# Kernel tuning notes

Measured on AMD Instinct MI355X. Metric: run time of the kernel, lower is better.

Reference implementation:

```python
import jax, jax.numpy as jnp
import numpy as np

B, N_IN, N_OUT = 16, 7000, 28000
C_IN, C_OUT, S = 64, 64, 9
NNZ = 3 * N_OUT  # ~3 source verts per upsampled vert (barycentric)


def setup_inputs() -> dict:
    key = jax.random.key(0)
    k = jax.random.split(key, 6)
    x = jax.random.normal(k[0], (B, N_IN, C_IN), dtype=jnp.float32)
    values = jax.random.uniform(k[1], (NNZ,), dtype=jnp.float32)
    row = jax.random.randint(k[2], (NNZ,), 0, N_OUT)
    col = jax.random.randint(k[3], (NNZ,), 0, N_IN)
    spiral_indices = jax.random.randint(k[4], (N_OUT, S), 0, N_OUT)
    weight = jax.random.normal(k[5], (S * C_IN, C_OUT), dtype=jnp.float32) * 0.02
    bias = jnp.zeros((C_OUT,), dtype=jnp.float32)
    return {"x": x, "values": values, "weight": weight, "bias": bias,
            "row": row, "col": col, "spiral_indices": spiral_indices}


def reference(x, values, weight, bias, row, col, spiral_indices):
    # Pool: gather source verts, scale by sparse matrix values, scatter-add to output verts
    n_out = spiral_indices.shape[0]
    gathered = x[:, col, :] * values[None, :, None]            # [B, nnz, C]
    pooled = jnp.zeros((x.shape[0], n_out, x.shape[2]), x.dtype).at[:, row, :].add(gathered)  # [B, N_out, C]
    # SpiralConv: gather spiral neighborhood, flatten, linear
    feat = pooled[:, spiral_indices.reshape(-1), :]            # [B, N_out*S, C]
    feat = feat.reshape(x.shape[0], n_out, -1)                 # [B, N_out, S*C]
    out = jax.nn.elu(jnp.einsum('bnf,fo->bno', feat, weight) + bias)
    return out
```

## Files before the change

kernel.cpp:

```cpp
#include <hip/hip_runtime.h>
#include <math.h>

#define B      16
#define N_IN   7000
#define N_OUT  28000
#define C      64
#define S      9
#define NNZ    (3 * N_OUT)
#define F      (S * C)
#define KB     (F / 32)

typedef short bf16x8 __attribute__((ext_vector_type(8)));
typedef float f32x4  __attribute__((ext_vector_type(4)));

static __device__ __forceinline__ unsigned short f2bf(float f) {
    unsigned u = __float_as_uint(f);
    u += 0x7fffu + ((u >> 16) & 1u);
    return (unsigned short)(u >> 16);
}

__global__ void hist_kernel(const int* __restrict__ row, int* __restrict__ cnt) {
    int i = blockIdx.x * 256 + threadIdx.x;
    if (i < NNZ) atomicAdd(&cnt[row[i]], 1);
}

__global__ void scan_kernel(const int* __restrict__ cnt,
                            int* __restrict__ offs, int* __restrict__ cursor) {
    __shared__ int tmp[1024];
    const int t = threadIdx.x;
    const int base = t * 28;
    const bool live = (t < 1000);

    int c[28];
    int partial = 0;
    if (live) {
        #pragma unroll
        for (int j = 0; j < 28; ++j) { c[j] = cnt[base + j]; partial += c[j]; }
    }
    tmp[t] = partial;
    __syncthreads();
    #pragma unroll
    for (int off = 1; off < 1024; off <<= 1) {
        int v = (t >= off) ? tmp[t - off] : 0;
        __syncthreads();
        tmp[t] += v;
        __syncthreads();
    }
    if (live) {
        int run = tmp[t] - partial;
        #pragma unroll
        for (int j = 0; j < 28; ++j) {
            offs[base + j]   = run;
            cursor[base + j] = run;
            run += c[j];
        }
        if (t == 999) offs[N_OUT] = run;
    }
}

__global__ void place_kernel(const int* __restrict__ row, const int* __restrict__ col,
                             const float* __restrict__ values,
                             int* __restrict__ cursor,
                             int* __restrict__ ecol, float* __restrict__ eval) {
    int i = blockIdx.x * 256 + threadIdx.x;
    if (i < NNZ) {
        int pos = atomicAdd(&cursor[row[i]], 1);
        ecol[pos] = col[i];
        eval[pos] = values[i];
    }
}

__global__ void pool_kernel(const float* __restrict__ x,
                            const int*   __restrict__ ecol,
                            const float* __restrict__ eval,
                            const int*   __restrict__ offs,
                            unsigned short* __restrict__ pooled) {
    const int bg     = blockIdx.x & 7;
    const int rowblk = blockIdx.x >> 3;
    const int wave = threadIdx.x >> 6;
    const int lane = threadIdx.x & 63;
    const int rsub = lane >> 5;
    const int bsub = (lane >> 4) & 1;
    const int sl   = lane & 15;

    const int r = rowblk * 8 + wave * 2 + rsub;
    const int b = bg + 8 * bsub;

    const int start = offs[r], end = offs[r + 1];

    float4 acc = make_float4(0.f, 0.f, 0.f, 0.f);
    const float* xb = x + (size_t)b * N_IN * C + sl * 4;

    for (int e = start; e < end; e += 4) {
        const int nn = end - e;
        int   cl[4]; float vv[4];
        #pragma unroll
        for (int j = 0; j < 4; ++j) {
            const int ee = (j < nn) ? e + j : e;
            cl[j] = ecol[ee];
            vv[j] = (j < nn) ? eval[ee] : 0.f;
        }
        float4 xv[4];
        #pragma unroll
        for (int j = 0; j < 4; ++j)
            xv[j] = *(const float4*)(xb + (size_t)cl[j] * C);
        #pragma unroll
        for (int j = 0; j < 4; ++j) {
            acc.x = fmaf(xv[j].x, vv[j], acc.x);
            acc.y = fmaf(xv[j].y, vv[j], acc.y);
            acc.z = fmaf(xv[j].z, vv[j], acc.z);
            acc.w = fmaf(xv[j].w, vv[j], acc.w);
        }
    }

    unsigned long long ov =
        (unsigned long long)f2bf(acc.x)
        | ((unsigned long long)f2bf(acc.y) << 16)
        | ((unsigned long long)f2bf(acc.z) << 32)
        | ((unsigned long long)f2bf(acc.w) << 48);
    unsigned short* dst = pooled + (size_t)bsub * (N_OUT * 512)
                        + (size_t)r * 512 + bg * 64 + sl * 4;
    __builtin_nontemporal_store(ov, (unsigned long long*)dst);
}

__global__ void packw_kernel(const float* __restrict__ w, unsigned short* __restrict__ pw) {
    const int kb   = blockIdx.x;
    const int nt   = threadIdx.x >> 6;
    const int lane = threadIdx.x & 63;
    const int lm   = lane & 15;
    const int quad = lane >> 4;

    unsigned short v[8];
    #pragma unroll
    for (int j = 0; j < 8; ++j) {
        const int k = kb * 32 + quad * 8 + j;
        const int n = nt * 16 + lm;
        v[j] = f2bf(w[(size_t)k * C + n]);
    }
    unsigned short* dst = pw + ((size_t)(kb * 4 + nt) * 64 + lane) * 8;
    #pragma unroll
    for (int j = 0; j < 8; ++j) dst[j] = v[j];
}

__global__ __launch_bounds__(512, 2)
void spiral_mfma(const unsigned short* __restrict__ pooled,
                 const bf16x8*         __restrict__ packedW,
                 const int*            __restrict__ sp,
                 const float*          __restrict__ bias,
                 float*                __restrict__ out) {
    const int Lb    = blockIdx.x;
    const int g     = Lb & 1;
    const int mtile = Lb >> 1;
    const int wave  = threadIdx.x >> 6;
    const int lane  = threadIdx.x & 63;
    const int lm    = lane & 15;
    const int quad  = lane >> 4;
    const int m_base = mtile * 32;
    const int b      = g * 8 + wave;

    __shared__ bf16x8         bw[KB * 4 * 64];
    __shared__ unsigned short apool[2][32][512];

    {
        const int t = threadIdx.x;
        #pragma unroll
        for (int i = 0; i < 9; ++i)
            bw[i * 512 + t] = packedW[i * 512 + t];
    }

    int spv[S];
    {
        const int r = m_base + (lane & 31);
        #pragma unroll
        for (int s = 0; s < S; ++s) spv[s] = sp[r * S + s];
    }

    const unsigned short* pgbase = pooled + (size_t)g * (N_OUT * 512);

    f32x4 acc[2][4];
    #pragma unroll
    for (int t = 0; t < 2; ++t)
        #pragma unroll
        for (int nt = 0; nt < 4; ++nt)
            acc[t][nt] = (f32x4){0.f, 0.f, 0.f, 0.f};

    bf16x8 ld[4];

    #pragma unroll
    for (int q = 0; q < 4; ++q) {
        const int r = __shfl(spv[0], wave * 4 + q, 64);
        ld[q] = *(const bf16x8*)(pgbase + (size_t)r * 512 + lane * 8);
    }
    #pragma unroll
    for (int q = 0; q < 4; ++q) {
        const int j = wave * 4 + q;
        *(bf16x8*)(&apool[0][j][(lane ^ (j & 7)) * 8]) = ld[q];
    }
    __syncthreads();

    #pragma unroll
    for (int s = 0; s < S; ++s) {
        const int cur = s & 1, nxt = cur ^ 1;

        if (s + 1 < S) {
            #pragma unroll
            for (int q = 0; q < 4; ++q) {
                const int r = __shfl(spv[s + 1], wave * 4 + q, 64);
                ld[q] = *(const bf16x8*)(pgbase + (size_t)r * 512 + lane * 8);
            }
        }

        #pragma unroll
        for (int half = 0; half < 2; ++half) {
            bf16x8 bb[4];
            #pragma unroll
            for (int nt = 0; nt < 4; ++nt)
                bb[nt] = bw[((s * 2 + half) * 4 + nt) * 64 + lane];
            bf16x8 aa[2];
            #pragma unroll
            for (int t = 0; t < 2; ++t) {
                const int j = t * 16 + lm;
                const int chunk = wave * 8 + (((half * 4 + quad) ^ (j & 7)));
                aa[t] = *(const bf16x8*)(&apool[cur][j][chunk * 8]);
            }
            #pragma unroll
            for (int nt = 0; nt < 4; ++nt)
                #pragma unroll
                for (int t = 0; t < 2; ++t)
                    acc[t][nt] = __builtin_amdgcn_mfma_f32_16x16x32_bf16(
                        aa[t], bb[nt], acc[t][nt], 0, 0, 0);
        }

        if (s + 1 < S) {
            #pragma unroll
            for (int q = 0; q < 4; ++q) {
                const int j = wave * 4 + q;
                *(bf16x8*)(&apool[nxt][j][(lane ^ (j & 7)) * 8]) = ld[q];
            }
        }
        __syncthreads();
    }

    #pragma unroll
    for (int nt = 0; nt < 4; ++nt) {
        const int n = nt * 16 + lm;
        const float bs = bias[n];
        #pragma unroll
        for (int t = 0; t < 2; ++t) {
            #pragma unroll
            for (int reg = 0; reg < 4; ++reg) {
                const int r = m_base + t * 16 + quad * 4 + reg;
                float v = acc[t][nt][reg] + bs;
                v = v > 0.f ? v : (__expf(v) - 1.0f);
                __builtin_nontemporal_store(v,
                    out + ((size_t)b * N_OUT + r) * C + n);
            }
        }
    }
}

extern "C" void kernel_launch(void* const* d_in, const int* in_sizes, int n_in,
                              void* d_out, int out_size, void* d_ws, size_t ws_size,
                              hipStream_t stream) {
    const float* x      = (const float*)d_in[0];
    const float* values = (const float*)d_in[1];
    const float* weight = (const float*)d_in[2];
    const float* bias   = (const float*)d_in[3];
    const int*   row    = (const int*)d_in[4];
    const int*   col    = (const int*)d_in[5];
    const int*   sp     = (const int*)d_in[6];
    float*       out    = (float*)d_out;

    char* ws = (char*)d_ws;
    size_t off = 0;
    unsigned short* pooled  = (unsigned short*)(ws + off); off += (size_t)B * N_OUT * C * 2;
    unsigned short* packedW = (unsigned short*)(ws + off); off += (size_t)KB * 4 * 64 * 8 * 2;
    int*   offs   = (int*)(ws + off); off += ((size_t)(N_OUT + 1) * 4 + 124) / 128 * 128;
    int*   cursor = (int*)(ws + off); off += (size_t)N_OUT * 4 + 128;
    int*   cnt    = (int*)(ws + off); off += (size_t)N_OUT * 4 + 128;
    int*   ecol   = (int*)(ws + off); off += (size_t)NNZ * 4;
    float* eval   = (float*)(ws + off); off += (size_t)NNZ * 4;

    (void)hipMemsetAsync(cnt, 0, (size_t)N_OUT * 4, stream);
    hist_kernel <<<(NNZ + 255) / 256, 256, 0, stream>>>(row, cnt);
    scan_kernel <<<1, 1024, 0, stream>>>(cnt, offs, cursor);
    place_kernel<<<(NNZ + 255) / 256, 256, 0, stream>>>(row, col, values, cursor, ecol, eval);

    packw_kernel<<<KB, 256, 0, stream>>>(weight, packedW);

    pool_kernel<<<3500 * 8, 256, 0, stream>>>(x, ecol, eval, offs, pooled);

    spiral_mfma<<<875 * 2, 512, 0, stream>>>(pooled,
        reinterpret_cast<const bf16x8*>(packedW), sp, bias, out);
}
```

Before: 300.3 us.

## Convert x to bf16 before pooling and stream weights per spiral step

Adds a kernel that converts x to bf16 so the pooling gather reads half the bytes. In the spiral GEMM, the full weight matrix is no longer held in LDS; one 8KB slice per spiral step is double-buffered alongside the A tiles, which shrinks LDS use so launch bounds can ask for 4 blocks per CU. The cost is an extra launch plus a full read and write of x, and weight slices now come from global memory every step. It also loses some pooled precision because inputs are rounded to bf16 before accumulation.

```diff
diff --git a/kernel.cpp b/kernel.cpp
--- a/kernel.cpp
+++ b/kernel.cpp
@@ -17,6 +17,9 @@
     unsigned u = __float_as_uint(f);
     u += 0x7fffu + ((u >> 16) & 1u);
     return (unsigned short)(u >> 16);
+}
+static __device__ __forceinline__ float bf2f(unsigned short s) {
+    return __uint_as_float((unsigned)s << 16);
 }
 
 __global__ void hist_kernel(const int* __restrict__ row, int* __restrict__ cnt) {
@@ -70,7 +73,18 @@
     }
 }
 
-__global__ void pool_kernel(const float* __restrict__ x,
+__global__ void xbf_kernel(const float* __restrict__ x, unsigned short* __restrict__ xb) {
+    const size_t i = ((size_t)blockIdx.x * 256 + threadIdx.x) * 8;
+    const float4 a = *(const float4*)(x + i);
+    const float4 c = *(const float4*)(x + i + 4);
+    ushort4 o0, o1;
+    o0.x = f2bf(a.x); o0.y = f2bf(a.y); o0.z = f2bf(a.z); o0.w = f2bf(a.w);
+    o1.x = f2bf(c.x); o1.y = f2bf(c.y); o1.z = f2bf(c.z); o1.w = f2bf(c.w);
+    *(ushort4*)(xb + i)     = o0;
+    *(ushort4*)(xb + i + 4) = o1;
+}
+
+__global__ void pool_kernel(const unsigned short* __restrict__ xb,
                             const int*   __restrict__ ecol,
                             const float* __restrict__ eval,
                             const int*   __restrict__ offs,
@@ -89,7 +103,7 @@
     const int start = offs[r], end = offs[r + 1];
 
     float4 acc = make_float4(0.f, 0.f, 0.f, 0.f);
-    const float* xb = x + (size_t)b * N_IN * C + sl * 4;
+    const unsigned short* xbb = xb + (size_t)b * N_IN * C + sl * 4;
 
     for (int e = start; e < end; e += 4) {
         const int nn = end - e;
@@ -100,16 +114,16 @@
             cl[j] = ecol[ee];
             vv[j] = (j < nn) ? eval[ee] : 0.f;
         }
-        float4 xv[4];
+        ushort4 xv[4];
         #pragma unroll
         for (int j = 0; j < 4; ++j)
-            xv[j] = *(const float4*)(xb + (size_t)cl[j] * C);
+            xv[j] = *(const ushort4*)(xbb + (size_t)cl[j] * C);
         #pragma unroll
         for (int j = 0; j < 4; ++j) {
-            acc.x = fmaf(xv[j].x, vv[j], acc.x);
-            acc.y = fmaf(xv[j].y, vv[j], acc.y);
-            acc.z = fmaf(xv[j].z, vv[j], acc.z);
-            acc.w = fmaf(xv[j].w, vv[j], acc.w);
+            acc.x = fmaf(bf2f(xv[j].x), vv[j], acc.x);
+            acc.y = fmaf(bf2f(xv[j].y), vv[j], acc.y);
+            acc.z = fmaf(bf2f(xv[j].z), vv[j], acc.z);
+            acc.w = fmaf(bf2f(xv[j].w), vv[j], acc.w);
         }
     }
 
@@ -142,7 +156,7 @@
     for (int j = 0; j < 8; ++j) dst[j] = v[j];
 }
 
-__global__ __launch_bounds__(512, 2)
+__global__ __launch_bounds__(512, 4)
 void spiral_mfma(const unsigned short* __restrict__ pooled,
                  const bf16x8*         __restrict__ packedW,
                  const int*            __restrict__ sp,
@@ -151,22 +165,16 @@
     const int Lb    = blockIdx.x;
     const int g     = Lb & 1;
     const int mtile = Lb >> 1;
-    const int wave  = threadIdx.x >> 6;
-    const int lane  = threadIdx.x & 63;
+    const int tid   = threadIdx.x;
+    const int wave  = tid >> 6;
+    const int lane  = tid & 63;
     const int lm    = lane & 15;
     const int quad  = lane >> 4;
     const int m_base = mtile * 32;
     const int b      = g * 8 + wave;
 
-    __shared__ bf16x8         bw[KB * 4 * 64];
     __shared__ unsigned short apool[2][32][512];
-
-    {
-        const int t = threadIdx.x;
-        #pragma unroll
-        for (int i = 0; i < 9; ++i)
-            bw[i * 512 + t] = packedW[i * 512 + t];
-    }
+    __shared__ bf16x8         bstage[2][512];
 
     int spv[S];
     {
@@ -184,18 +192,21 @@
         for (int nt = 0; nt < 4; ++nt)
             acc[t][nt] = (f32x4){0.f, 0.f, 0.f, 0.f};
 
-    bf16x8 ld[4];
+    bf16x8 ldA[4];
+    bf16x8 ldB;
 
     #pragma unroll
     for (int q = 0; q < 4; ++q) {
         const int r = __shfl(spv[0], wave * 4 + q, 64);
-        ld[q] = *(const bf16x8*)(pgbase + (size_t)r * 512 + lane * 8);
-    }
+        ldA[q] = *(const bf16x8*)(pgbase + (size_t)r * 512 + lane * 8);
+    }
+    ldB = packedW[tid];
     #pragma unroll
     for (int q = 0; q < 4; ++q) {
         const int j = wave * 4 + q;
-        *(bf16x8*)(&apool[0][j][(lane ^ (j & 7)) * 8]) = ld[q];
-    }
+        *(bf16x8*)(&apool[0][j][(lane ^ (j & 7)) * 8]) = ldA[q];
+    }
+    bstage[0][tid] = ldB;
     __syncthreads();
 
     #pragma unroll
@@ -206,8 +217,9 @@
             #pragma unroll
             for (int q = 0; q < 4; ++q) {
                 const int r = __shfl(spv[s + 1], wave * 4 + q, 64);
-                ld[q] = *(const bf16x8*)(pgbase + (size_t)r * 512 + lane * 8);
+                ldA[q] = *(const bf16x8*)(pgbase + (size_t)r * 512 + lane * 8);
             }
+            ldB = packedW[(s + 1) * 512 + tid];
         }
 
         #pragma unroll
@@ -215,7 +227,7 @@
             bf16x8 bb[4];
             #pragma unroll
             for (int nt = 0; nt < 4; ++nt)
-                bb[nt] = bw[((s * 2 + half) * 4 + nt) * 64 + lane];
+                bb[nt] = bstage[cur][(half * 4 + nt) * 64 + lane];
             bf16x8 aa[2];
             #pragma unroll
             for (int t = 0; t < 2; ++t) {
@@ -235,8 +247,9 @@
             #pragma unroll
             for (int q = 0; q < 4; ++q) {
                 const int j = wave * 4 + q;
-                *(bf16x8*)(&apool[nxt][j][(lane ^ (j & 7)) * 8]) = ld[q];
+                *(bf16x8*)(&apool[nxt][j][(lane ^ (j & 7)) * 8]) = ldA[q];
             }
+            bstage[nxt][tid] = ldB;
         }
         __syncthreads();
     }
@@ -275,6 +288,7 @@
     size_t off = 0;
     unsigned short* pooled  = (unsigned short*)(ws + off); off += (size_t)B * N_OUT * C * 2;
     unsigned short* packedW = (unsigned short*)(ws + off); off += (size_t)KB * 4 * 64 * 8 * 2;
+    unsigned short* xbf     = (unsigned short*)(ws + off); off += (size_t)B * N_IN * C * 2;
     int*   offs   = (int*)(ws + off); off += ((size_t)(N_OUT + 1) * 4 + 124) / 128 * 128;
     int*   cursor = (int*)(ws + off); off += (size_t)N_OUT * 4 + 128;
     int*   cnt    = (int*)(ws + off); off += (size_t)N_OUT * 4 + 128;
@@ -288,7 +302,9 @@
 
     packw_kernel<<<KB, 256, 0, stream>>>(weight, packedW);
 
-    pool_kernel<<<3500 * 8, 256, 0, stream>>>(x, ecol, eval, offs, pooled);
+    xbf_kernel<<<3500, 256, 0, stream>>>(x, xbf);
+
+    pool_kernel<<<3500 * 8, 256, 0, stream>>>(xbf, ecol, eval, offs, pooled);
 
     spiral_mfma<<<875 * 2, 512, 0, stream>>>(pooled,
         reinterpret_cast<const bf16x8*>(packedW), sp, bias, out);
```

Measured after the change: 296.3 us. No clear change (-1.4%).
